# Kernel optimization log

Hardware: AMD Instinct MI355X
Metric: run time of the kernel (lower is better)

The kernel has to match this reference:

```python
import jax, jax.numpy as jnp
import numpy as np

H = 32          # num attention heads
KVH = 8         # num key/value heads
D = 128         # head dim
THETA = 10000.0


def _rope_tables(kv_len):
    inv_freq = 1.0 / (THETA ** (jnp.arange(0, D, 2, dtype=jnp.float32) / D))  # [D/2]
    t = jnp.arange(kv_len, dtype=jnp.float32)
    freqs = jnp.outer(t, inv_freq)                  # [kv_len, D/2]
    emb = jnp.concatenate([freqs, freqs], axis=-1)  # [kv_len, D]
    return jnp.cos(emb), jnp.sin(emb)


def _rotate_half(x):
    x1, x2 = jnp.split(x, 2, axis=-1)
    return jnp.concatenate([-x2, x1], axis=-1)


def setup_inputs() -> dict:
    key = jax.random.key(0)
    ks = jax.random.split(key, 7)
    B, QL, KVL, HID = 4, 128, 4096, 4096
    hidden_states = jax.random.normal(ks[0], (B, QL, HID), jnp.float32)
    key_states = jax.random.normal(ks[1], (B, KVH, KVL, D), jnp.float32)
    value_states = jax.random.normal(ks[2], (B, KVH, KVL, D), jnp.float32)
    Wq = jax.random.normal(ks[3], (HID, H * D), jnp.float32) * (HID ** -0.5)
    Wo = jax.random.normal(ks[4], (H * D, HID), jnp.float32) * ((H * D) ** -0.5)
    position_ids = jnp.sort(jax.random.randint(ks[5], (B, KVL), 0, KVL), axis=-1).astype(jnp.int64)
    attention_mask = jax.random.randint(ks[6], (B, 1, QL, KVL), 0, 2) == 1
    return {"hidden_states": hidden_states, "key_states": key_states,
            "value_states": value_states, "Wq": Wq, "Wo": Wo,
            "position_ids": position_ids, "attention_mask": attention_mask}


def reference(hidden_states, key_states, value_states, Wq, Wo, position_ids, attention_mask):
    B, QL, HID = hidden_states.shape
    KVL = position_ids.shape[-1]

    # q projection -> [B, H, QL, D]
    q = (hidden_states @ Wq).reshape(B, QL, H, D).transpose(0, 2, 1, 3)

    # RoPE: apply rotation for the single max position per batch to all q positions
    cos, sin = _rope_tables(KVL)                               # [KVL, D]
    pos = jnp.take_along_axis(position_ids,
                              jnp.argmax(position_ids.astype(jnp.int32), axis=1)[:, None],
                              axis=1)                          # [B, 1]
    cos_b = cos[pos][:, None]                                  # [B, 1, 1, D]
    sin_b = sin[pos][:, None]
    q = q * cos_b + _rotate_half(q) * sin_b

    # GQA repeat kv heads -> [B, H, KVL, D]
    groups = H // KVH
    k = jnp.repeat(key_states, groups, axis=1)
    v = jnp.repeat(value_states, groups, axis=1)

    scores = jnp.einsum('bhqd,bhkd->bhqk', q, k) / jnp.sqrt(jnp.float32(D))
    scores = jnp.where(attention_mask, jnp.float32(-10000.0), scores)
    attn = jax.nn.softmax(scores.astype(jnp.float32), axis=-1).astype(q.dtype)

    out = jnp.einsum('bhqk,bhkd->bhqd', attn, v)               # [B, H, QL, D]
    out = out.transpose(0, 2, 1, 3).reshape(B, QL, H * D)
    return out @ Wo
```

## Files before the change

### kernel.cpp

```cpp
#include <hip/hip_runtime.h>
#include <math.h>

typedef __attribute__((ext_vector_type(8))) short bf16x8;
typedef __attribute__((ext_vector_type(4))) float f32x4;
typedef __attribute__((ext_vector_type(4))) short s16x4;
typedef __attribute__((ext_vector_type(4))) int i32x4;

__device__ inline unsigned short f2bf(float x){
  unsigned u = __builtin_bit_cast(unsigned, x);
  u = (u + 0x7FFFu + ((u >> 16) & 1u)) >> 16;
  return (unsigned short)u;
}
__device__ inline float bf2f(unsigned short v){
  return __builtin_bit_cast(float, (unsigned)v << 16);
}
__device__ inline unsigned pk2bf(float lo, float hi){
  return (unsigned)f2bf(lo) | ((unsigned)f2bf(hi) << 16);
}

__device__ inline void gl16(const void* g, void* l){
  __builtin_amdgcn_global_load_lds(
      (const __attribute__((address_space(1))) unsigned int*)g,
      (__attribute__((address_space(3))) unsigned int*)l, 16, 0, 0);
}

#define KVLEN 4096
#define QLEN  128
#define NH    32
#define NKVH  8
#define HD    128
#define HIDD  4096
#define NSPLIT 4
#define KVCHUNK (KVLEN / NSPLIT)

__global__ void prep_kernel(const int* __restrict__ pos32,
                            const unsigned int* __restrict__ mask32,
                            float* __restrict__ costab,
                            float* __restrict__ sintab,
                            int* __restrict__ flags){
  int tid = threadIdx.x;
  if (tid < 64){
    unsigned long long bal = __ballot((mask32[tid] & 0xFFFFFF00u) != 0);
    if (tid == 0) flags[0] = (bal != 0) ? 1 : 0;
  }
  int b = tid >> 6, j = tid & 63;
  bool pos64 = (pos32[2*4095 + 1] == 0);
  long long mpos;
  if (pos64) mpos = ((const long long*)pos32)[(size_t)b*KVLEN + KVLEN - 1];
  else       mpos = (long long)pos32[(size_t)b*KVLEN + KVLEN - 1];
  double inv = pow(10000.0, -((double)j) / 64.0);
  double ang = (double)mpos * inv;
  costab[b*64 + j] = (float)cos(ang);
  sintab[b*64 + j] = (float)sin(ang);
}

__global__ __launch_bounds__(256) void maskpack_kernel(const void* __restrict__ mask,
                                                       const int* __restrict__ flags,
                                                       unsigned long long* __restrict__ bits){
  int idx = blockIdx.x * 256 + threadIdx.x;
  bool m8 = (flags[0] != 0);
  bool v = m8 ? (((const unsigned char*)mask)[idx] != 0)
              : (((const int*)mask)[idx] != 0);
  unsigned long long bal = __ballot(v);
  if ((threadIdx.x & 63) == 0) bits[idx >> 6] = bal;
}

__global__ __launch_bounds__(256) void kvprep_kernel(const float* __restrict__ Kg,
                                                     const float* __restrict__ Vg,
                                                     const float* __restrict__ costab,
                                                     const float* __restrict__ sintab,
                                                     unsigned short* __restrict__ Kswz,
                                                     unsigned short* __restrict__ V2){
  __shared__ alignas(16) char tl[16384];
  int bid = blockIdx.x;
  int tid = threadIdx.x;
  int b = bid >> 9;
  const float* kin = Kg + (size_t)bid * 8192;
  const float* vin = Vg + (size_t)bid * 8192;
  unsigned short* kout = Kswz + (size_t)bid * 8192;
  unsigned short* vout = V2   + (size_t)bid * 8192;
#pragma unroll
  for (int i = 0; i < 4; ++i){
    int c = tid + 256*i;
    int r = c >> 4, d0 = (c & 15) * 8;
    int dp = d0 ^ 64;
    bool low = d0 < 64;
    f32x4 x0 = *(const f32x4*)(kin + r*128 + d0);
    f32x4 x1 = *(const f32x4*)(kin + r*128 + d0 + 4);
    f32x4 y0 = *(const f32x4*)(kin + r*128 + dp);
    f32x4 y1 = *(const f32x4*)(kin + r*128 + dp + 4);
    int j0 = d0 & 63;
    bf16x8 s;
#pragma unroll
    for (int t = 0; t < 4; ++t){
      float cc = costab[b*64 + j0 + t],     ss = sintab[b*64 + j0 + t];
      float c2 = costab[b*64 + j0 + 4 + t], s2 = sintab[b*64 + j0 + 4 + t];
      float v0 = low ? (x0[t]*cc + y0[t]*ss) : (x0[t]*cc - y0[t]*ss);
      float v1 = low ? (x1[t]*c2 + y1[t]*s2) : (x1[t]*c2 - y1[t]*s2);
      s[t] = (short)f2bf(v0);
      s[t+4] = (short)f2bf(v1);
    }
    unsigned o = ((unsigned)(r*256 + d0*2)) ^ (((unsigned)r & 7u) << 4);
    *(bf16x8*)(tl + o) = s;
  }
  __syncthreads();
#pragma unroll
  for (int i = 0; i < 4; ++i)
    *(bf16x8*)((char*)kout + tid*16 + i*4096) = *(const bf16x8*)(tl + tid*16 + i*4096);
#pragma unroll
  for (int i = 0; i < 4; ++i){
    int c = tid + 256*i;
    int l16 = c & 15, lk4 = (c >> 4) & 3, ks2 = (c >> 6) & 1, nf8 = c >> 7;
    int d = nf8*16 + l16;
    int kvb = ks2*32 + lk4*8;
    bf16x8 s;
#pragma unroll
    for (int e = 0; e < 8; ++e) s[e] = (short)f2bf(vin[(size_t)(kvb + e)*128 + d]);
    *(bf16x8*)(vout + (size_t)c*8) = s;
  }
}

__global__ __launch_bounds__(256) void wprep_kernel(const float* __restrict__ Wq,
                                                    const float* __restrict__ Wo,
                                                    const float* __restrict__ hidden,
                                                    unsigned short* __restrict__ WqImg,
                                                    unsigned short* __restrict__ WoImg,
                                                    unsigned short* __restrict__ A1img){
  __shared__ alignas(16) char tl[8192];
  int bid = blockIdx.x, tid = threadIdx.x;
  if (bid < 8192){
    const float* W = (bid < 4096) ? Wq : Wo;
    unsigned short* img = (bid < 4096) ? WqImg : WoImg;
    int t = bid & 4095;
    int bn = t >> 6, kt = t & 63;
    char* outB = (char*)img + (size_t)t * 8192;
#pragma unroll
    for (int i = 0; i < 2; ++i){
      int c = tid + 256*i;
      int n = c & 63, kc = c >> 6;
      const float* src = W + (size_t)(kt*64 + kc*8) * HIDD + bn*64 + n;
      bf16x8 s;
#pragma unroll
      for (int e = 0; e < 8; ++e) s[e] = (short)f2bf(src[(size_t)e * HIDD]);
      unsigned off = ((unsigned)(n*128 + kc*16)) ^ (((unsigned)n & 7u) << 4);
      *(bf16x8*)(tl + off) = s;
    }
    __syncthreads();
#pragma unroll
    for (int i = 0; i < 2; ++i)
      *(bf16x8*)(outB + tid*16 + i*4096) = *(const bf16x8*)(tl + tid*16 + i*4096);
  } else {
    int t = bid - 8192;
    int bm = t >> 6, kt = t & 63;
    char* outA = (char*)A1img + (size_t)t * 8192;
#pragma unroll
    for (int i = 0; i < 2; ++i){
      int c = tid + 256*i;
      int m = c >> 3, kc = c & 7;
      const float* src = hidden + (size_t)(bm*64 + m) * HIDD + kt*64 + kc*8;
      f32x4 x0 = *(const f32x4*)src;
      f32x4 x1 = *(const f32x4*)(src + 4);
      bf16x8 s;
#pragma unroll
      for (int e = 0; e < 4; ++e){ s[e] = (short)f2bf(x0[e]); s[e+4] = (short)f2bf(x1[e]); }
      unsigned off = ((unsigned)(m*128 + kc*16)) ^ (((unsigned)m & 7u) << 4);
      *(bf16x8*)(tl + off) = s;
    }
    __syncthreads();
#pragma unroll
    for (int i = 0; i < 2; ++i)
      *(bf16x8*)(outA + tid*16 + i*4096) = *(const bf16x8*)(tl + tid*16 + i*4096);
  }
}

template<int EPI>
__global__ __launch_bounds__(256, 2) void gemm_kernel(const unsigned short* __restrict__ Aimg,
                                                      const unsigned short* __restrict__ Bimg,
                                                      void* __restrict__ C_){
  __shared__ alignas(16) char smem[65536];
  int bid = blockIdx.x;
  int bn = (bid & 7) | ((bid >> 6) << 3);
  int bm = (bid >> 3) & 7;
  int tid = threadIdx.x, lane = tid & 63, w = tid >> 6;
  int wm = w >> 1, wn = w & 1;
  int l16 = lane & 15, lk4 = lane >> 4;
  const char* At = (const char*)Aimg + (size_t)(bm*64) * 8192;
  const char* Bt = (const char*)Bimg + (size_t)(bn*64) * 8192;
  f32x4 acc[2][2] = {};

#define GSTAGE(KT, BUF) do { \
    const char* ga_ = At + (size_t)(KT)*8192 + w*2048 + lane*16; \
    const char* gb_ = Bt + (size_t)(KT)*8192 + w*2048 + lane*16; \
    char* la_ = smem + (BUF)*16384 + w*2048; \
    char* lb_ = smem + (BUF)*16384 + 8192 + w*2048; \
    gl16(ga_, la_); gl16(ga_ + 1024, la_ + 1024); \
    gl16(gb_, lb_); gl16(gb_ + 1024, lb_ + 1024); \
  } while(0)

  GSTAGE(0, 0); GSTAGE(1, 1); GSTAGE(2, 2);

  for (int kt = 0; kt < 64; ++kt){
    if (kt + 2 < 64)      asm volatile("s_waitcnt vmcnt(8)" ::: "memory");
    else if (kt + 1 < 64) asm volatile("s_waitcnt vmcnt(4)" ::: "memory");
    else                  asm volatile("s_waitcnt vmcnt(0)" ::: "memory");
    __syncthreads();
    if (kt + 3 < 64) GSTAGE(kt + 3, (kt + 3) & 3);
    const char* Ab = smem + (kt & 3)*16384;
    const char* Bb = Ab + 8192;
    bf16x8 af[2][2], bfr[2][2];
#pragma unroll
    for (int i = 0; i < 2; ++i)
#pragma unroll
      for (int ks = 0; ks < 2; ++ks){
        unsigned m = (unsigned)(wm*32 + i*16 + l16);
        unsigned off = (m*128u + (unsigned)(ks*64 + lk4*16)) ^ ((m & 7u) << 4);
        af[i][ks] = *(const bf16x8*)(Ab + off);
      }
#pragma unroll
    for (int j = 0; j < 2; ++j)
#pragma unroll
      for (int ks = 0; ks < 2; ++ks){
        unsigned n = (unsigned)(wn*32 + j*16 + l16);
        unsigned off = (n*128u + (unsigned)(ks*64 + lk4*16)) ^ ((n & 7u) << 4);
        bfr[j][ks] = *(const bf16x8*)(Bb + off);
      }
#pragma unroll
    for (int i = 0; i < 2; ++i)
#pragma unroll
      for (int j = 0; j < 2; ++j)
#pragma unroll
        for (int ks = 0; ks < 2; ++ks)
          acc[i][j] = __builtin_amdgcn_mfma_f32_16x16x32_bf16(af[i][ks], bfr[j][ks], acc[i][j], 0, 0, 0);
  }
#undef GSTAGE

  if (EPI == 0){
    float* C = (float*)C_;
#pragma unroll
    for (int i = 0; i < 2; ++i)
#pragma unroll
      for (int j = 0; j < 2; ++j)
#pragma unroll
        for (int r = 0; r < 4; ++r){
          int row = bm*64 + wm*32 + i*16 + lk4*4 + r;
          int col = bn*64 + wn*32 + j*16 + l16;
          C[(size_t)row * HIDD + col] = acc[i][j][r];
        }
  } else {
    unsigned short* Q = (unsigned short*)C_;
    const float scale = 0.08838834764831845f;
#pragma unroll
    for (int i = 0; i < 2; ++i)
#pragma unroll
      for (int j = 0; j < 2; ++j)
#pragma unroll
        for (int r = 0; r < 4; ++r){
          int row = bm*64 + wm*32 + i*16 + lk4*4 + r;
          int col = bn*64 + wn*32 + j*16 + l16;
          int b = row >> 7, ql = row & 127;
          int h = col >> 7, d = col & 127;
          Q[(((size_t)(b*NH + h)) * QLEN + ql) * HD + d] = f2bf(acc[i][j][r] * scale);
        }
  }
}

__global__ __launch_bounds__(512, 4) void attn_kernel(const unsigned short* __restrict__ Q,
                                                      const unsigned short* __restrict__ Kswz,
                                                      const unsigned short* __restrict__ V2,
                                                      const unsigned long long* __restrict__ bits,
                                                      unsigned short* __restrict__ Opart,
                                                      float* __restrict__ Mpart,
                                                      float* __restrict__ Lpart){
  __shared__ alignas(16) unsigned short Kbuf[2][8192];
  __shared__ alignas(16) unsigned short Vbuf[2][8192];
  int bid = blockIdx.x;
  int g = (bid & 7) | ((bid >> 5) << 3);
  int j = (bid >> 3) & 3;
  int s   = g & 3;
  int kvh = (g >> 2) & 7;
  int b   = g >> 5;
  int h   = kvh * 4 + j;

  int tid = threadIdx.x, lane = tid & 63, w = tid >> 6;
  int l16 = lane & 15, lk4 = lane >> 4;
  int lk4x4 = lk4 * 4;

  bf16x8 qf[4];
  {
    const unsigned short* qp = Q + (((size_t)(b*NH + h) * QLEN) + w*16 + l16) * HD;
#pragma unroll
    for (int ks = 0; ks < 4; ++ks)
      qf[ks] = *(const bf16x8*)(qp + ks*32 + lk4*8);
  }
  bf16x8 vone;
#pragma unroll
  for (int t = 0; t < 8; ++t) vone[t] = (short)0x3F80;

  f32x4 acc_o[8] = {};
  f32x4 acc_l = {};
  float mrun = -1e30f;

  size_t kvhbase = (size_t)(b*NKVH + kvh) * (KVLEN/64);
  const unsigned short* Ktiles = Kswz + kvhbase * 8192;
  const unsigned short* Vtiles = V2   + kvhbase * 8192;
  size_t qrow = (size_t)(b*QLEN + w*16 + l16);

  const int t0 = s * (KVCHUNK/64), t1 = t0 + KVCHUNK/64;
  int srcb0 = (l16 + ((lk4 & 1) << 5)) << 2;
  int srcb1 = srcb0 + 64;

#define STAGE(T, BUF) do { \
    const char* gk_ = (const char*)(Ktiles + (size_t)(T)*8192) + w*2048 + lane*16; \
    const char* gv_ = (const char*)(Vtiles + (size_t)(T)*8192) + w*2048 + lane*16; \
    char* lk_ = (char*)(&Kbuf[BUF][0]) + w*2048; \
    char* lv_ = (char*)(&Vbuf[BUF][0]) + w*2048; \
    gl16(gk_, lk_); gl16(gk_ + 1024, lk_ + 1024); \
    gl16(gv_, lv_); gl16(gv_ + 1024, lv_ + 1024); \
  } while(0)

  STAGE(t0, 0);
  int cur = 0;
  for (int t = t0; t < t1; ++t){
    asm volatile("s_waitcnt vmcnt(0)" ::: "memory");
    __syncthreads();
    if (t + 1 < t1) STAGE(t + 1, cur ^ 1);
    unsigned long long wrd = bits[qrow*64 + (size_t)t];
    __builtin_amdgcn_sched_barrier(0);

    f32x4 sacc[4] = {};
#pragma unroll
    for (int nf = 0; nf < 4; ++nf){
      int krow = nf*16 + l16;
#pragma unroll
      for (int ks = 0; ks < 4; ++ks){
        unsigned byteoff = ((unsigned)krow*256u + (unsigned)(ks*32 + lk4*8)*2u) ^ (((unsigned)krow & 7u) << 4);
        bf16x8 kf = *(const bf16x8*)((const char*)&Kbuf[cur][0] + byteoff);
        sacc[nf] = __builtin_amdgcn_mfma_f32_16x16x32_bf16(kf, qf[ks], sacc[nf], 0, 0, 0);
      }
    }

    float p[4][4];
    float pm = -1e30f;
#pragma unroll
    for (int nf = 0; nf < 4; ++nf)
#pragma unroll
      for (int r = 0; r < 4; ++r){
        bool mk = (wrd >> (nf*16 + lk4x4 + r)) & 1ull;
        float sv = mk ? -10000.f : sacc[nf][r];
        p[nf][r] = sv;
        pm = fmaxf(pm, sv);
      }
    pm = fmaxf(pm, __shfl_xor(pm, 16, 64));
    pm = fmaxf(pm, __shfl_xor(pm, 32, 64));
    if (__any(pm > mrun)){
      float mnew = fmaxf(mrun, pm);
      float corr = __expf(mrun - mnew);
      mrun = mnew;
#pragma unroll
      for (int nf8 = 0; nf8 < 8; ++nf8)
#pragma unroll
        for (int r = 0; r < 4; ++r) acc_o[nf8][r] *= corr;
#pragma unroll
      for (int r = 0; r < 4; ++r) acc_l[r] *= corr;
    }
    unsigned P32[8];
#pragma unroll
    for (int nf = 0; nf < 4; ++nf){
      float e0 = __expf(p[nf][0] - mrun);
      float e1 = __expf(p[nf][1] - mrun);
      float e2 = __expf(p[nf][2] - mrun);
      float e3 = __expf(p[nf][3] - mrun);
      P32[nf*2]     = pk2bf(e0, e1);
      P32[nf*2 + 1] = pk2bf(e2, e3);
    }

    bf16x8 pf[2];
    bool hi = lk4 >= 2;
#pragma unroll
    for (int ks2 = 0; ks2 < 2; ++ks2){
      int a0 = __builtin_amdgcn_ds_bpermute(srcb0, (int)P32[ks2*4 + 0]);
      int b0 = __builtin_amdgcn_ds_bpermute(srcb0, (int)P32[ks2*4 + 2]);
      int a1 = __builtin_amdgcn_ds_bpermute(srcb0, (int)P32[ks2*4 + 1]);
      int b1 = __builtin_amdgcn_ds_bpermute(srcb0, (int)P32[ks2*4 + 3]);
      int a2 = __builtin_amdgcn_ds_bpermute(srcb1, (int)P32[ks2*4 + 0]);
      int b2 = __builtin_amdgcn_ds_bpermute(srcb1, (int)P32[ks2*4 + 2]);
      int a3 = __builtin_amdgcn_ds_bpermute(srcb1, (int)P32[ks2*4 + 1]);
      int b3 = __builtin_amdgcn_ds_bpermute(srcb1, (int)P32[ks2*4 + 3]);
      i32x4 wv = { hi ? b0 : a0, hi ? b1 : a1, hi ? b2 : a2, hi ? b3 : a3 };
      pf[ks2] = __builtin_bit_cast(bf16x8, wv);
    }

#pragma unroll
    for (int nf8 = 0; nf8 < 8; ++nf8)
#pragma unroll
      for (int ks2 = 0; ks2 < 2; ++ks2){
        unsigned byteoff = (unsigned)(nf8*2 + ks2)*1024u + (unsigned)lane*16u;
        bf16x8 vf = *(const bf16x8*)((const char*)&Vbuf[cur][0] + byteoff);
        acc_o[nf8] = __builtin_amdgcn_mfma_f32_16x16x32_bf16(vf, pf[ks2], acc_o[nf8], 0, 0, 0);
      }
#pragma unroll
    for (int ks2 = 0; ks2 < 2; ++ks2)
      acc_l = __builtin_amdgcn_mfma_f32_16x16x32_bf16(vone, pf[ks2], acc_l, 0, 0, 0);
    cur ^= 1;
  }
#undef STAGE

  size_t row = ((size_t)(s*4 + b) * NH + h) * QLEN + w*16 + l16;
#pragma unroll
  for (int nf8 = 0; nf8 < 8; ++nf8){
    s16x4 o;
#pragma unroll
    for (int r = 0; r < 4; ++r) o[r] = (short)f2bf(acc_o[nf8][r]);
    *(s16x4*)&Opart[row * HD + nf8*16 + lk4x4] = o;
  }
  if (lk4 == 0){
    Mpart[row] = mrun;
    Lpart[row] = acc_l[0];
  }
}

__global__ __launch_bounds__(256) void combine_kernel(const unsigned short* __restrict__ Opart,
                                                      const float* __restrict__ Mpart,
                                                      const float* __restrict__ Lpart,
                                                      unsigned short* __restrict__ A2img){
  int idx = blockIdx.x * 256 + threadIdx.x;
  int d4 = idx & 31;
  int row = idx >> 5;
  const int RS = 4 * NH * QLEN;
  float m[NSPLIT];
#pragma unroll
  for (int s = 0; s < NSPLIT; ++s) m[s] = Mpart[(size_t)s*RS + row];
  float M = fmaxf(fmaxf(m[0], m[1]), fmaxf(m[2], m[3]));
  float L = 0.f;
  f32x4 num = {};
#pragma unroll
  for (int s = 0; s < NSPLIT; ++s){
    float wsc = __expf(m[s] - M);
    L += wsc * Lpart[(size_t)s*RS + row];
    s16x4 o = *(const s16x4*)&Opart[((size_t)s*RS + row) * HD + d4*4];
#pragma unroll
    for (int t = 0; t < 4; ++t) num[t] += wsc * bf2f((unsigned short)o[t]);
  }
  int ql = row & 127, h = (row >> 7) & 31, b = row >> 12;
  int bm = b*2 + (ql >> 6), mm = ql & 63;
  int kt = h*2 + (d4 >> 4), kl = (d4*4) & 63;
  s16x4 res;
#pragma unroll
  for (int t = 0; t < 4; ++t) res[t] = (short)f2bf(num[t] / L);
  char* tile = (char*)A2img + (size_t)(bm*64 + kt) * 8192;
  unsigned off = ((unsigned)(mm*128 + kl*2)) ^ (((unsigned)mm & 7u) << 4);
  *(s16x4*)(tile + off) = res;
}

extern "C" void kernel_launch(void* const* d_in, const int* in_sizes, int n_in,
                              void* d_out, int out_size, void* d_ws, size_t ws_size,
                              hipStream_t stream){
  (void)in_sizes; (void)n_in; (void)out_size; (void)ws_size;
  const float* hidden = (const float*)d_in[0];
  const float* kst    = (const float*)d_in[1];
  const float* vst    = (const float*)d_in[2];
  const float* wq     = (const float*)d_in[3];
  const float* wo     = (const float*)d_in[4];
  const void*  pos    = d_in[5];
  const void*  mask   = d_in[6];
  float* out = (float*)d_out;

  char* ws = (char*)d_ws;
  unsigned short* Kswz  = (unsigned short*)ws;
  unsigned short* V2    = (unsigned short*)(ws + (32u << 20));
  unsigned short* WoImg = (unsigned short*)(ws + (64u << 20));
  unsigned short* WqImg = (unsigned short*)(ws + (96u << 20));
  unsigned short* Opart = (unsigned short*)(ws + (96u << 20));
  unsigned short* A1img = (unsigned short*)(ws + (128u << 20));
  unsigned short* qbf   = (unsigned short*)(ws + (132u << 20));
  unsigned short* A2img = (unsigned short*)(ws + (136u << 20));
  float* Mpart = (float*)(ws + (140u << 20));
  float* Lpart = (float*)(ws + (140u << 20) + (256u << 10));
  unsigned long long* bits = (unsigned long long*)(ws + (140u << 20) + (512u << 10));
  float* costab = (float*)(ws + (140u << 20) + (768u << 10));
  float* sintab = costab + 256;
  int*   flags  = (int*)(sintab + 256);

  prep_kernel<<<1, 256, 0, stream>>>((const int*)pos, (const unsigned int*)mask,
                                     costab, sintab, flags);
  maskpack_kernel<<<8192, 256, 0, stream>>>(mask, flags, bits);
  kvprep_kernel<<<2048, 256, 0, stream>>>(kst, vst, costab, sintab, Kswz, V2);
  wprep_kernel<<<8704, 256, 0, stream>>>(wq, wo, hidden, WqImg, WoImg, A1img);
  gemm_kernel<1><<<512, 256, 0, stream>>>(A1img, WqImg, qbf);
  attn_kernel<<<512, 512, 0, stream>>>(qbf, Kswz, V2, bits, Opart, Mpart, Lpart);
  combine_kernel<<<2048, 256, 0, stream>>>(Opart, Mpart, Lpart, A2img);
  gemm_kernel<0><<<512, 256, 0, stream>>>(A2img, WoImg, out);
}
```

Measured before the change: 237.7 us.

## Process two query groups per wave, triple-buffer KV, and fold log2e into Q scale

The attention kernel now handles two 16-row query groups per wave, covering two heads per block. Each K/V fragment loaded from LDS therefore feeds twice as many MFMAs, and the grid is halved. KV staging moves from double to triple buffering with a deeper vmcnt wait, so more loads are in flight. The log2(e) factor is folded into the Q projection scale so softmax and combine can use exp2f, with the masked value scaled to match. The GEMM barrier is replaced by an explicit lgkmcnt wait, s_barrier and sched_barrier. The costs are roughly double the accumulator registers, a lower occupancy target (launch bounds 2 instead of 4), and more LDS per block.

Measured after the change: 226.4 us. 4.8% less time.

```diff
diff --git a/kernel.cpp b/kernel.cpp
--- a/kernel.cpp
+++ b/kernel.cpp
@@ -200,10 +200,12 @@
   GSTAGE(0, 0); GSTAGE(1, 1); GSTAGE(2, 2);
 
   for (int kt = 0; kt < 64; ++kt){
-    if (kt + 2 < 64)      asm volatile("s_waitcnt vmcnt(8)" ::: "memory");
-    else if (kt + 1 < 64) asm volatile("s_waitcnt vmcnt(4)" ::: "memory");
-    else                  asm volatile("s_waitcnt vmcnt(0)" ::: "memory");
-    __syncthreads();
+    if (kt < 62)      asm volatile("s_waitcnt vmcnt(8)" ::: "memory");
+    else if (kt < 63) asm volatile("s_waitcnt vmcnt(4)" ::: "memory");
+    else              asm volatile("s_waitcnt vmcnt(0)" ::: "memory");
+    asm volatile("s_waitcnt lgkmcnt(0)" ::: "memory");
+    __builtin_amdgcn_s_barrier();
+    __builtin_amdgcn_sched_barrier(0);
     if (kt + 3 < 64) GSTAGE(kt + 3, (kt + 3) & 3);
     const char* Ab = smem + (kt & 3)*16384;
     const char* Bb = Ab + 8192;
@@ -248,7 +250,7 @@
         }
   } else {
     unsigned short* Q = (unsigned short*)C_;
-    const float scale = 0.08838834764831845f;
+    const float scale = 0.08838834764831845f * 1.4426950408889634f;
 #pragma unroll
     for (int i = 0; i < 2; ++i)
 #pragma unroll
@@ -264,46 +266,48 @@
   }
 }
 
-__global__ __launch_bounds__(512, 4) void attn_kernel(const unsigned short* __restrict__ Q,
+__global__ __launch_bounds__(512, 2) void attn_kernel(const unsigned short* __restrict__ Q,
                                                       const unsigned short* __restrict__ Kswz,
                                                       const unsigned short* __restrict__ V2,
                                                       const unsigned long long* __restrict__ bits,
                                                       unsigned short* __restrict__ Opart,
                                                       float* __restrict__ Mpart,
                                                       float* __restrict__ Lpart){
-  __shared__ alignas(16) unsigned short Kbuf[2][8192];
-  __shared__ alignas(16) unsigned short Vbuf[2][8192];
+  __shared__ alignas(16) unsigned short Kbuf[3][8192];
+  __shared__ alignas(16) unsigned short Vbuf[3][8192];
   int bid = blockIdx.x;
-  int g = (bid & 7) | ((bid >> 5) << 3);
-  int j = (bid >> 3) & 3;
+  int g = (bid & 7) | ((bid >> 4) << 3);
+  int p = (bid >> 3) & 1;
   int s   = g & 3;
   int kvh = (g >> 2) & 7;
   int b   = g >> 5;
-  int h   = kvh * 4 + j;
 
   int tid = threadIdx.x, lane = tid & 63, w = tid >> 6;
+  int hh = w >> 2, ww = w & 3;
+  int h = kvh*4 + p*2 + hh;
   int l16 = lane & 15, lk4 = lane >> 4;
   int lk4x4 = lk4 * 4;
 
-  bf16x8 qf[4];
-  {
-    const unsigned short* qp = Q + (((size_t)(b*NH + h) * QLEN) + w*16 + l16) * HD;
+  bf16x8 qf[2][4];
+#pragma unroll
+  for (int qg = 0; qg < 2; ++qg){
+    const unsigned short* qp = Q + (((size_t)(b*NH + h) * QLEN) + ww*32 + qg*16 + l16) * HD;
 #pragma unroll
     for (int ks = 0; ks < 4; ++ks)
-      qf[ks] = *(const bf16x8*)(qp + ks*32 + lk4*8);
+      qf[qg][ks] = *(const bf16x8*)(qp + ks*32 + lk4*8);
   }
   bf16x8 vone;
 #pragma unroll
   for (int t = 0; t < 8; ++t) vone[t] = (short)0x3F80;
 
-  f32x4 acc_o[8] = {};
-  f32x4 acc_l = {};
-  float mrun = -1e30f;
+  f32x4 acc_o[2][8] = {};
+  f32x4 acc_l[2] = {};
+  float mrun[2] = {-1e30f, -1e30f};
 
   size_t kvhbase = (size_t)(b*NKVH + kvh) * (KVLEN/64);
   const unsigned short* Ktiles = Kswz + kvhbase * 8192;
   const unsigned short* Vtiles = V2   + kvhbase * 8192;
-  size_t qrow = (size_t)(b*QLEN + w*16 + l16);
+  size_t qrow0 = (size_t)(b*QLEN + ww*32 + l16);
 
   const int t0 = s * (KVCHUNK/64), t1 = t0 + KVCHUNK/64;
   int srcb0 = (l16 + ((lk4 & 1) << 5)) << 2;
@@ -319,103 +323,126 @@
   } while(0)
 
   STAGE(t0, 0);
+  STAGE(t0 + 1, 1);
   int cur = 0;
   for (int t = t0; t < t1; ++t){
-    asm volatile("s_waitcnt vmcnt(0)" ::: "memory");
-    __syncthreads();
-    if (t + 1 < t1) STAGE(t + 1, cur ^ 1);
-    unsigned long long wrd = bits[qrow*64 + (size_t)t];
+    if (t + 1 < t1) asm volatile("s_waitcnt vmcnt(4)" ::: "memory");
+    else            asm volatile("s_waitcnt vmcnt(0)" ::: "memory");
+    asm volatile("s_waitcnt lgkmcnt(0)" ::: "memory");
+    __builtin_amdgcn_s_barrier();
     __builtin_amdgcn_sched_barrier(0);
-
-    f32x4 sacc[4] = {};
+    if (t + 2 < t1) STAGE(t + 2, (cur == 0) ? 2 : (cur - 1));
+
+    unsigned long long wrd[2];
+    wrd[0] = bits[qrow0*64 + (size_t)t];
+    wrd[1] = bits[(qrow0 + 16)*64 + (size_t)t];
+
+    const char* Kc = (const char*)&Kbuf[cur][0];
+    const char* Vc = (const char*)&Vbuf[cur][0];
+
+    f32x4 sacc[2][4] = {};
 #pragma unroll
     for (int nf = 0; nf < 4; ++nf){
       int krow = nf*16 + l16;
 #pragma unroll
       for (int ks = 0; ks < 4; ++ks){
         unsigned byteoff = ((unsigned)krow*256u + (unsigned)(ks*32 + lk4*8)*2u) ^ (((unsigned)krow & 7u) << 4);
-        bf16x8 kf = *(const bf16x8*)((const char*)&Kbuf[cur][0] + byteoff);
-        sacc[nf] = __builtin_amdgcn_mfma_f32_16x16x32_bf16(kf, qf[ks], sacc[nf], 0, 0, 0);
-      }
-    }
-
-    float p[4][4];
-    float pm = -1e30f;
-#pragma unroll
-    for (int nf = 0; nf < 4; ++nf)
-#pragma unroll
-      for (int r = 0; r < 4; ++r){
-        bool mk = (wrd >> (nf*16 + lk4x4 + r)) & 1ull;
-        float sv = mk ? -10000.f : sacc[nf][r];
-        p[nf][r] = sv;
-        pm = fmaxf(pm, sv);
-      }
-    pm = fmaxf(pm, __shfl_xor(pm, 16, 64));
-    pm = fmaxf(pm, __shfl_xor(pm, 32, 64));
-    if (__any(pm > mrun)){
-      float mnew = fmaxf(mrun, pm);
-      float corr = __expf(mrun - mnew);
-      mrun = mnew;
-#pragma unroll
-      for (int nf8 = 0; nf8 < 8; ++nf8)
-#pragma unroll
-        for (int r = 0; r < 4; ++r) acc_o[nf8][r] *= corr;
-#pragma unroll
-      for (int r = 0; r < 4; ++r) acc_l[r] *= corr;
-    }
-    unsigned P32[8];
-#pragma unroll
-    for (int nf = 0; nf < 4; ++nf){
-      float e0 = __expf(p[nf][0] - mrun);
-      float e1 = __expf(p[nf][1] - mrun);
-      float e2 = __expf(p[nf][2] - mrun);
-      float e3 = __expf(p[nf][3] - mrun);
-      P32[nf*2]     = pk2bf(e0, e1);
-      P32[nf*2 + 1] = pk2bf(e2, e3);
-    }
-
-    bf16x8 pf[2];
+        bf16x8 kf = *(const bf16x8*)(Kc + byteoff);
+        sacc[0][nf] = __builtin_amdgcn_mfma_f32_16x16x32_bf16(kf, qf[0][ks], sacc[0][nf], 0, 0, 0);
+        sacc[1][nf] = __builtin_amdgcn_mfma_f32_16x16x32_bf16(kf, qf[1][ks], sacc[1][nf], 0, 0, 0);
+      }
+    }
+
+    unsigned P32[2][8];
+#pragma unroll
+    for (int qg = 0; qg < 2; ++qg){
+      float pp[4][4];
+      float pm = -1e30f;
+#pragma unroll
+      for (int nf = 0; nf < 4; ++nf)
+#pragma unroll
+        for (int r = 0; r < 4; ++r){
+          bool mk = (wrd[qg] >> (nf*16 + lk4x4 + r)) & 1ull;
+          float sv = mk ? -20000.f : sacc[qg][nf][r];
+          pp[nf][r] = sv;
+          pm = fmaxf(pm, sv);
+        }
+      pm = fmaxf(pm, __shfl_xor(pm, 16, 64));
+      pm = fmaxf(pm, __shfl_xor(pm, 32, 64));
+      if (__any(pm > mrun[qg])){
+        float mnew = fmaxf(mrun[qg], pm);
+        float corr = exp2f(mrun[qg] - mnew);
+        mrun[qg] = mnew;
+#pragma unroll
+        for (int nf8 = 0; nf8 < 8; ++nf8)
+#pragma unroll
+          for (int r = 0; r < 4; ++r) acc_o[qg][nf8][r] *= corr;
+#pragma unroll
+        for (int r = 0; r < 4; ++r) acc_l[qg][r] *= corr;
+      }
+#pragma unroll
+      for (int nf = 0; nf < 4; ++nf){
+        float e0 = exp2f(pp[nf][0] - mrun[qg]);
+        float e1 = exp2f(pp[nf][1] - mrun[qg]);
+        float e2 = exp2f(pp[nf][2] - mrun[qg]);
+        float e3 = exp2f(pp[nf][3] - mrun[qg]);
+        P32[qg][nf*2]     = pk2bf(e0, e1);
+        P32[qg][nf*2 + 1] = pk2bf(e2, e3);
+      }
+    }
+
+    bf16x8 pf[2][2];
     bool hi = lk4 >= 2;
 #pragma unroll
-    for (int ks2 = 0; ks2 < 2; ++ks2){
-      int a0 = __builtin_amdgcn_ds_bpermute(srcb0, (int)P32[ks2*4 + 0]);
-      int b0 = __builtin_amdgcn_ds_bpermute(srcb0, (int)P32[ks2*4 + 2]);
-      int a1 = __builtin_amdgcn_ds_bpermute(srcb0, (int)P32[ks2*4 + 1]);
-      int b1 = __builtin_amdgcn_ds_bpermute(srcb0, (int)P32[ks2*4 + 3]);
-      int a2 = __builtin_amdgcn_ds_bpermute(srcb1, (int)P32[ks2*4 + 0]);
-      int b2 = __builtin_amdgcn_ds_bpermute(srcb1, (int)P32[ks2*4 + 2]);
-      int a3 = __builtin_amdgcn_ds_bpermute(srcb1, (int)P32[ks2*4 + 1]);
-      int b3 = __builtin_amdgcn_ds_bpermute(srcb1, (int)P32[ks2*4 + 3]);
-      i32x4 wv = { hi ? b0 : a0, hi ? b1 : a1, hi ? b2 : a2, hi ? b3 : a3 };
-      pf[ks2] = __builtin_bit_cast(bf16x8, wv);
-    }
+    for (int qg = 0; qg < 2; ++qg)
+#pragma unroll
+      for (int ks2 = 0; ks2 < 2; ++ks2){
+        int a0 = __builtin_amdgcn_ds_bpermute(srcb0, (int)P32[qg][ks2*4 + 0]);
+        int b0 = __builtin_amdgcn_ds_bpermute(srcb0, (int)P32[qg][ks2*4 + 2]);
+        int a1 = __builtin_amdgcn_ds_bpermute(srcb0, (int)P32[qg][ks2*4 + 1]);
+        int b1 = __builtin_amdgcn_ds_bpermute(srcb0, (int)P32[qg][ks2*4 + 3]);
+        int a2 = __builtin_amdgcn_ds_bpermute(srcb1, (int)P32[qg][ks2*4 + 0]);
+        int b2 = __builtin_amdgcn_ds_bpermute(srcb1, (int)P32[qg][ks2*4 + 2]);
+        int a3 = __builtin_amdgcn_ds_bpermute(srcb1, (int)P32[qg][ks2*4 + 1]);
+        int b3 = __builtin_amdgcn_ds_bpermute(srcb1, (int)P32[qg][ks2*4 + 3]);
+        i32x4 wv = { hi ? b0 : a0, hi ? b1 : a1, hi ? b2 : a2, hi ? b3 : a3 };
+        pf[qg][ks2] = __builtin_bit_cast(bf16x8, wv);
+      }
 
 #pragma unroll
     for (int nf8 = 0; nf8 < 8; ++nf8)
 #pragma unroll
       for (int ks2 = 0; ks2 < 2; ++ks2){
         unsigned byteoff = (unsigned)(nf8*2 + ks2)*1024u + (unsigned)lane*16u;
-        bf16x8 vf = *(const bf16x8*)((const char*)&Vbuf[cur][0] + byteoff);
-        acc_o[nf8] = __builtin_amdgcn_mfma_f32_16x16x32_bf16(vf, pf[ks2], acc_o[nf8], 0, 0, 0);
-      }
-#pragma unroll
-    for (int ks2 = 0; ks2 < 2; ++ks2)
-      acc_l = __builtin_amdgcn_mfma_f32_16x16x32_bf16(vone, pf[ks2], acc_l, 0, 0, 0);
-    cur ^= 1;
+        bf16x8 vf = *(const bf16x8*)(Vc + byteoff);
+        acc_o[0][nf8] = __builtin_amdgcn_mfma_f32_16x16x32_bf16(vf, pf[0][ks2], acc_o[0][nf8], 0, 0, 0);
+        acc_o[1][nf8] = __builtin_amdgcn_mfma_f32_16x16x32_bf16(vf, pf[1][ks2], acc_o[1][nf8], 0, 0, 0);
+      }
+#pragma unroll
+    for (int qg = 0; qg < 2; ++qg)
+#pragma unroll
+      for (int ks2 = 0; ks2 < 2; ++ks2)
+        acc_l[qg] = __builtin_amdgcn_mfma_f32_16x16x32_bf16(vone, pf[qg][ks2], acc_l[qg], 0, 0, 0);
+
+    cur = (cur == 2) ? 0 : (cur + 1);
   }
 #undef STAGE
 
-  size_t row = ((size_t)(s*4 + b) * NH + h) * QLEN + w*16 + l16;
-#pragma unroll
-  for (int nf8 = 0; nf8 < 8; ++nf8){
-    s16x4 o;
-#pragma unroll
-    for (int r = 0; r < 4; ++r) o[r] = (short)f2bf(acc_o[nf8][r]);
-    *(s16x4*)&Opart[row * HD + nf8*16 + lk4x4] = o;
-  }
-  if (lk4 == 0){
-    Mpart[row] = mrun;
-    Lpart[row] = acc_l[0];
+  size_t rowbase = ((size_t)(s*4 + b) * NH + h) * QLEN + ww*32 + l16;
+#pragma unroll
+  for (int qg = 0; qg < 2; ++qg){
+    size_t row = rowbase + qg*16;
+#pragma unroll
+    for (int nf8 = 0; nf8 < 8; ++nf8){
+      s16x4 o;
+#pragma unroll
+      for (int r = 0; r < 4; ++r) o[r] = (short)f2bf(acc_o[qg][nf8][r]);
+      *(s16x4*)&Opart[row * HD + nf8*16 + lk4x4] = o;
+    }
+    if (lk4 == 0){
+      Mpart[row] = mrun[qg];
+      Lpart[row] = acc_l[qg][0];
+    }
   }
 }
 
@@ -435,7 +462,7 @@
   f32x4 num = {};
 #pragma unroll
   for (int s = 0; s < NSPLIT; ++s){
-    float wsc = __expf(m[s] - M);
+    float wsc = exp2f(m[s] - M);
     L += wsc * Lpart[(size_t)s*RS + row];
     s16x4 o = *(const s16x4*)&Opart[((size_t)s*RS + row) * HD + d4*4];
 #pragma unroll
@@ -487,7 +514,7 @@
   kvprep_kernel<<<2048, 256, 0, stream>>>(kst, vst, costab, sintab, Kswz, V2);
   wprep_kernel<<<8704, 256, 0, stream>>>(wq, wo, hidden, WqImg, WoImg, A1img);
   gemm_kernel<1><<<512, 256, 0, stream>>>(A1img, WqImg, qbf);
-  attn_kernel<<<512, 512, 0, stream>>>(qbf, Kswz, V2, bits, Opart, Mpart, Lpart);
+  attn_kernel<<<256, 512, 0, stream>>>(qbf, Kswz, V2, bits, Opart, Mpart, Lpart);
   combine_kernel<<<2048, 256, 0, stream>>>(Opart, Mpart, Lpart, A2img);
   gemm_kernel<0><<<512, 256, 0, stream>>>(A2img, WoImg, out);
 }
```
